# Kernel optimization log

Measured on AMD Instinct MI355X. Metric: run time of the kernel, lower is better.

Reference implementation:

```python
import jax, jax.numpy as jnp
import numpy as np

B, T, N = 1024, 128, 5
HIDDEN = 160
FML = HIDDEN // N            # 32, per-node state width
FC = (256, 256, 512)
IN_F = (FML + 1) * N         # 165: full graph -> every node sees all 5 nodes
N_CLASSES = 7
BN_EPS = 1e-5


def setup_inputs() -> dict:
    key = jax.random.key(0)
    ks = jax.random.split(key, 12)
    init = lambda k, sh: (jax.random.normal(k, sh, jnp.float32) * 0.02)
    return {
        "x": jax.random.normal(ks[0], (B, N, T), jnp.float32),
        # per-node 3-layer MLP f_i, stacked over nodes
        "Wf1": init(ks[1], (N, IN_F, FC[0])), "bf1": jnp.zeros((N, FC[0]), jnp.float32),
        "Wf2": init(ks[2], (N, FC[0], FC[1])), "bf2": jnp.zeros((N, FC[1]), jnp.float32),
        "Wf3": init(ks[3], (N, FC[1], FML)), "bf3": jnp.zeros((N, FML), jnp.float32),
        # output head: Linear -> ReLU -> BatchNorm1d -> Linear -> Softmax
        "Wo1": init(ks[4], (IN_F, FC[2])), "bo1": jnp.zeros((FC[2],), jnp.float32),
        "gamma": jnp.ones((FC[2],), jnp.float32), "beta": jnp.zeros((FC[2],), jnp.float32),
        "Wo2": init(ks[5], (FC[2], N_CLASSES)), "bo2": jnp.zeros((N_CLASSES,), jnp.float32),
    }


def reference(x, Wf1, bf1, Wf2, bf2, Wf3, bf3, Wo1, bo1, gamma, beta, Wo2, bo2):
    batch = x.shape[0]
    xt = jnp.transpose(x, (2, 0, 1))                  # [T, B, N]
    state0 = jnp.zeros((batch, N, FML), x.dtype)      # [B, N, FML]

    def step(state, x_t):
        # Gauss-Seidel update: node i sees states already updated this step
        for i in range(N):
            inp = jnp.concatenate([x_t, state.reshape(batch, -1)], axis=1)  # [B, 165]
            h = jax.nn.relu(inp @ Wf1[i] + bf1[i])
            h = jax.nn.relu(h @ Wf2[i] + bf2[i])
            s_i = jax.nn.relu(h @ Wf3[i] + bf3[i])    # [B, FML]
            state = state.at[:, i, :].set(s_i)
        return state, None

    state, _ = jax.lax.scan(step, state0, xt)
    feat = jnp.concatenate([xt[-1], state.reshape(batch, -1)], axis=1)       # [B, 165]
    h = jax.nn.relu(feat @ Wo1 + bo1)
    # BatchNorm1d in training mode: batch mean, biased batch variance
    mu = jnp.mean(h, axis=0)
    var = jnp.mean((h - mu) ** 2, axis=0)
    h = (h - mu) / jnp.sqrt(var + BN_EPS) * gamma + beta
    logits = h @ Wo2 + bo2
    return jax.nn.softmax(logits, axis=1)             # [B, 7]
```

## Files before the change

### kernel.cpp

```cpp
#include <hip/hip_runtime.h>
#include <hip/hip_bf16.h>

#define B_TOT 1024
#define T_STEPS 128
#define N_NODES 5
#define FML 32
#define IN_F 165
#define F1 256
#define F2 256
#define F3 512
#define NCLS 7
#define BM 16
#define BMH 8

typedef __attribute__((ext_vector_type(8))) short bfrag;
typedef __attribute__((ext_vector_type(4))) float f32x4;

#define MFMA16 __builtin_amdgcn_mfma_f32_16x16x32_bf16

#define L1_KT 6
#define L1_CT 16
#define L2_KT 8
#define L2_CT 16
#define L3_KT 8
#define L3_CT 2
#define L1_FRAGS (L1_KT * L1_CT)
#define L2_FRAGS (L2_KT * L2_CT)
#define L3_FRAGS (L3_KT * L3_CT)

#define INP_STRIDE 200
#define H_STRIDE 264

__device__ __forceinline__ __hip_bfloat16 tobf(float v) { return __float2bfloat16(v); }

__device__ __forceinline__ void phase_barrier() {
  asm volatile("s_waitcnt lgkmcnt(0)" ::: "memory");
  __builtin_amdgcn_s_barrier();
  __builtin_amdgcn_sched_barrier(0);
}

__global__ __launch_bounds__(256) void pack_weights(
    const float* __restrict__ Wf1, const float* __restrict__ Wf2, const float* __restrict__ Wf3,
    __hip_bfloat16* __restrict__ p1, __hip_bfloat16* __restrict__ p2, __hip_bfloat16* __restrict__ p3) {
  int tid = blockIdx.x * 256 + threadIdx.x;
  int node = tid / (240 * 64);
  int rem  = tid % (240 * 64);
  int frag = rem >> 6;
  int lane = rem & 63;
  int g = lane >> 4, c16 = lane & 15;
  if (frag < L1_FRAGS) {
    int kt = frag / L1_CT, ct = frag % L1_CT;
    __hip_bfloat16* dst = p1 + (((size_t)node * L1_FRAGS + frag) * 64 + lane) * 8;
    const float* W = Wf1 + (size_t)node * IN_F * F1;
#pragma unroll
    for (int e = 0; e < 8; ++e) {
      int k = kt * 32 + g * 8 + e;
      int row = (k < 160) ? (5 + k) : ((k < IN_F) ? (k - 160) : -1);
      float v = (row >= 0) ? W[(size_t)row * F1 + ct * 16 + c16] : 0.f;
      dst[e] = tobf(v);
    }
  } else if (frag < L1_FRAGS + L2_FRAGS) {
    int f = frag - L1_FRAGS;
    __hip_bfloat16* dst = p2 + (((size_t)node * L2_FRAGS + f) * 64 + lane) * 8;
    const float* W = Wf2 + (size_t)node * F1 * F2;
    int kt = f / L2_CT, ct = f % L2_CT;
#pragma unroll
    for (int e = 0; e < 8; ++e) {
      int k = kt * 32 + g * 8 + e;
      dst[e] = tobf(W[(size_t)k * F2 + ct * 16 + c16]);
    }
  } else {
    int f = frag - L1_FRAGS - L2_FRAGS;
    __hip_bfloat16* dst = p3 + (((size_t)node * L3_FRAGS + f) * 64 + lane) * 8;
    const float* W = Wf3 + (size_t)node * F2 * FML;
    int kt = f / L3_CT, ct = f % L3_CT;
#pragma unroll
    for (int e = 0; e < 8; ++e) {
      int k = kt * 32 + g * 8 + e;
      dst[e] = tobf(W[(size_t)k * FML + ct * 16 + c16]);
    }
  }
}

__device__ __forceinline__ void relu_pack_store(__hip_bfloat16* p, f32x4 acc, float4 b) {
  union { ushort4 v; __hip_bfloat16 h[4]; } u;
  u.h[0] = tobf(fmaxf(acc[0] + b.x, 0.f));
  u.h[1] = tobf(fmaxf(acc[1] + b.y, 0.f));
  u.h[2] = tobf(fmaxf(acc[2] + b.z, 0.f));
  u.h[3] = tobf(fmaxf(acc[3] + b.w, 0.f));
  *reinterpret_cast<ushort4*>(p) = u.v;
}

__global__ __launch_bounds__(512, 2) void recur_kernel(
    const float* __restrict__ x,
    const __hip_bfloat16* __restrict__ p1, const float* __restrict__ bf1,
    const __hip_bfloat16* __restrict__ p2, const float* __restrict__ bf2,
    const __hip_bfloat16* __restrict__ p3, const float* __restrict__ bf3,
    float* __restrict__ feat_out) {
  __shared__ __align__(16) __hip_bfloat16 inp_s[BM][INP_STRIDE];
  __shared__ __align__(16) __hip_bfloat16 h1_s[BM][H_STRIDE];
  __shared__ __align__(16) __hip_bfloat16 h2_s[BM][H_STRIDE];
  __shared__ __align__(16) bfrag wf3_s[N_NODES * L3_FRAGS * 64];

  const int tid = threadIdx.x;
  const int lane = tid & 63;
  const int w = tid >> 6;
  const int g = lane >> 4;
  const int c16 = lane & 15;
  const int ct0 = 2 * w, ct1 = 2 * w + 1;
  const int r0 = blockIdx.x * BM;

  const bfrag* Pf1 = (const bfrag*)p1;
  const bfrag* Pf2 = (const bfrag*)p2;

  const bool xact = (tid >= 128 && tid < 128 + BM * N_NODES);
  const int xr = (tid - 128) / N_NODES, xn = (tid - 128) % N_NODES;

  {
    const uint4* src = (const uint4*)p3;
    uint4* dst = (uint4*)wf3_s;
    for (int i2 = tid; i2 < N_NODES * L3_FRAGS * 64; i2 += 512) dst[i2] = src[i2];
  }
  for (int idx = tid; idx < BM * INP_STRIDE; idx += 512)
    ((__hip_bfloat16*)inp_s)[idx] = tobf(0.f);
  __syncthreads();
  if (tid < BM * N_NODES) {
    int r = tid / N_NODES, n = tid % N_NODES;
    inp_s[r][160 + n] = tobf(x[(size_t)(r0 + r) * (N_NODES * T_STEPS) + n * T_STEPS]);
  }
  __syncthreads();

  bfrag wL1[2][L1_KT];
#pragma unroll
  for (int kt = 0; kt < L1_KT; ++kt) {
    wL1[0][kt] = Pf1[(kt * L1_CT + ct0) * 64 + lane];
    wL1[1][kt] = Pf1[(kt * L1_CT + ct1) * 64 + lane];
  }

#pragma unroll 1
  for (int t = 0; t < T_STEPS; ++t) {
#pragma unroll 1
    for (int i = 0; i < N_NODES; ++i) {
      const int inext = (i + 1 == N_NODES) ? 0 : i + 1;

      bfrag w2[2][L2_KT];
      {
        const bfrag* P = Pf2 + (size_t)i * L2_FRAGS * 64;
#pragma unroll
        for (int kt = 0; kt < L2_KT; ++kt) {
          w2[0][kt] = P[(kt * L2_CT + ct0) * 64 + lane];
          w2[1][kt] = P[(kt * L2_CT + ct1) * 64 + lane];
        }
      }
      float xv = 0.f;
      if (i == 0 && xact && t + 1 < T_STEPS)
        xv = x[(size_t)(r0 + xr) * (N_NODES * T_STEPS) + xn * T_STEPS + (t + 1)];

      {
        float4 bia0 = *(const float4*)&bf1[i * F1 + ct0 * 16 + 4 * g];
        float4 bia1 = *(const float4*)&bf1[i * F1 + ct1 * 16 + 4 * g];
        bfrag a[L1_KT];
#pragma unroll
        for (int kt = 0; kt < L1_KT; ++kt)
          a[kt] = *(const bfrag*)&inp_s[c16][kt * 32 + g * 8];
        f32x4 acc0 = {0.f,0.f,0.f,0.f}, acc1 = {0.f,0.f,0.f,0.f};
        f32x4 acc0b = {0.f,0.f,0.f,0.f}, acc1b = {0.f,0.f,0.f,0.f};
#pragma unroll
        for (int kt = 0; kt < 3; ++kt) {
          acc0  = MFMA16(wL1[0][kt],     a[kt],     acc0,  0, 0, 0);
          acc1  = MFMA16(wL1[1][kt],     a[kt],     acc1,  0, 0, 0);
          acc0b = MFMA16(wL1[0][kt + 3], a[kt + 3], acc0b, 0, 0, 0);
          acc1b = MFMA16(wL1[1][kt + 3], a[kt + 3], acc1b, 0, 0, 0);
        }
        acc0 += acc0b; acc1 += acc1b;
        relu_pack_store(&h1_s[c16][ct0 * 16 + 4 * g], acc0, bia0);
        relu_pack_store(&h1_s[c16][ct1 * 16 + 4 * g], acc1, bia1);
      }
      phase_barrier();

      bfrag w1n[2][L1_KT];
      {
        const bfrag* P = Pf1 + (size_t)inext * L1_FRAGS * 64;
#pragma unroll
        for (int kt = 0; kt < L1_KT; ++kt) {
          w1n[0][kt] = P[(kt * L1_CT + ct0) * 64 + lane];
          w1n[1][kt] = P[(kt * L1_CT + ct1) * 64 + lane];
        }
      }
      {
        float4 bib0 = *(const float4*)&bf2[i * F2 + ct0 * 16 + 4 * g];
        float4 bib1 = *(const float4*)&bf2[i * F2 + ct1 * 16 + 4 * g];
        bfrag ab[L2_KT];
#pragma unroll
        for (int kt = 0; kt < L2_KT; ++kt)
          ab[kt] = *(const bfrag*)&h1_s[c16][kt * 32 + g * 8];
        f32x4 bcc0 = {0.f,0.f,0.f,0.f}, bcc1 = {0.f,0.f,0.f,0.f};
        f32x4 bcc0b = {0.f,0.f,0.f,0.f}, bcc1b = {0.f,0.f,0.f,0.f};
#pragma unroll
        for (int kt = 0; kt < 4; ++kt) {
          bcc0  = MFMA16(w2[0][kt],     ab[kt],     bcc0,  0, 0, 0);
          bcc1  = MFMA16(w2[1][kt],     ab[kt],     bcc1,  0, 0, 0);
          bcc0b = MFMA16(w2[0][kt + 4], ab[kt + 4], bcc0b, 0, 0, 0);
          bcc1b = MFMA16(w2[1][kt + 4], ab[kt + 4], bcc1b, 0, 0, 0);
        }
        bcc0 += bcc0b; bcc1 += bcc1b;
        relu_pack_store(&h2_s[c16][ct0 * 16 + 4 * g], bcc0, bib0);
        relu_pack_store(&h2_s[c16][ct1 * 16 + 4 * g], bcc1, bib1);
      }
      phase_barrier();

      if (w < 2) {
        bfrag ac[L3_KT], wc[L3_KT];
#pragma unroll
        for (int kt = 0; kt < L3_KT; ++kt) {
          wc[kt] = wf3_s[((size_t)i * L3_FRAGS + kt * L3_CT + w) * 64 + lane];
          ac[kt] = *(const bfrag*)&h2_s[c16][kt * 32 + g * 8];
        }
        f32x4 ccc = {0.f,0.f,0.f,0.f}, cccb = {0.f,0.f,0.f,0.f};
#pragma unroll
        for (int kt = 0; kt < 4; ++kt) {
          ccc  = MFMA16(wc[kt],     ac[kt],     ccc,  0, 0, 0);
          cccb = MFMA16(wc[kt + 4], ac[kt + 4], cccb, 0, 0, 0);
        }
        ccc += cccb;
        const int sc = i * FML + w * 16 + 4 * g;
        float4 bic = *(const float4*)&bf3[sc];
        union { ushort4 v; __hip_bfloat16 h[4]; } u;
        float vs[4];
#pragma unroll
        for (int e = 0; e < 4; ++e) {
          vs[e] = fmaxf(ccc[e] + ((const float*)&bic)[e], 0.f);
          u.h[e] = tobf(vs[e]);
        }
        *reinterpret_cast<ushort4*>(&inp_s[c16][sc]) = u.v;
        if (t == T_STEPS - 1) {
#pragma unroll
          for (int e = 0; e < 4; ++e)
            feat_out[(size_t)(r0 + c16) * IN_F + 5 + sc + e] = vs[e];
        }
      } else if (i == N_NODES - 1 && xact && t + 1 < T_STEPS) {
        float xv2 = x[(size_t)(r0 + xr) * (N_NODES * T_STEPS) + xn * T_STEPS + (t + 1)];
        inp_s[xr][160 + xn] = tobf(xv2);
      }
      phase_barrier();

#pragma unroll
      for (int kt = 0; kt < L1_KT; ++kt) {
        wL1[0][kt] = w1n[0][kt];
        wL1[1][kt] = w1n[1][kt];
      }
    }
  }

  if (tid < BM * N_NODES) {
    int r = tid / N_NODES, n = tid % N_NODES;
    feat_out[(size_t)(r0 + r) * IN_F + n] =
        x[(size_t)(r0 + r) * (N_NODES * T_STEPS) + n * T_STEPS + (T_STEPS - 1)];
  }
}

__global__ __launch_bounds__(256) void head1_kernel(
    const float* __restrict__ feat, const float* __restrict__ Wo1,
    const float* __restrict__ bo1, float* __restrict__ H) {
  __shared__ __align__(16) float f[BMH][168];
  const int tid = threadIdx.x;
  const int r0 = blockIdx.x * BMH;
  for (int idx = tid; idx < BMH * 168; idx += 256) {
    int r = idx / 168, c = idx % 168;
    f[r][c] = (c < IN_F) ? feat[(size_t)(r0 + r) * IN_F + c] : 0.f;
  }
  __syncthreads();
  const int c0 = tid, c1 = tid + 256;
  float acc0[BMH], acc1[BMH];
#pragma unroll
  for (int r = 0; r < BMH; ++r) { acc0[r] = 0.f; acc1[r] = 0.f; }
  int k = 0;
  for (; k + 3 < IN_F; k += 4) {
    float w00 = Wo1[(k + 0) * F3 + c0], w01 = Wo1[(k + 0) * F3 + c1];
    float w10 = Wo1[(k + 1) * F3 + c0], w11 = Wo1[(k + 1) * F3 + c1];
    float w20 = Wo1[(k + 2) * F3 + c0], w21 = Wo1[(k + 2) * F3 + c1];
    float w30 = Wo1[(k + 3) * F3 + c0], w31 = Wo1[(k + 3) * F3 + c1];
#pragma unroll
    for (int r = 0; r < BMH; ++r) {
      float4 v = *reinterpret_cast<const float4*>(&f[r][k]);
      acc0[r] = fmaf(v.x, w00, acc0[r]); acc1[r] = fmaf(v.x, w01, acc1[r]);
      acc0[r] = fmaf(v.y, w10, acc0[r]); acc1[r] = fmaf(v.y, w11, acc1[r]);
      acc0[r] = fmaf(v.z, w20, acc0[r]); acc1[r] = fmaf(v.z, w21, acc1[r]);
      acc0[r] = fmaf(v.w, w30, acc0[r]); acc1[r] = fmaf(v.w, w31, acc1[r]);
    }
  }
  {
    float w0 = Wo1[164 * F3 + c0], w1 = Wo1[164 * F3 + c1];
#pragma unroll
    for (int r = 0; r < BMH; ++r) {
      acc0[r] = fmaf(f[r][164], w0, acc0[r]);
      acc1[r] = fmaf(f[r][164], w1, acc1[r]);
    }
  }
  float b0 = bo1[c0], b1 = bo1[c1];
#pragma unroll
  for (int r = 0; r < BMH; ++r) {
    H[(size_t)(r0 + r) * F3 + c0] = fmaxf(acc0[r] + b0, 0.f);
    H[(size_t)(r0 + r) * F3 + c1] = fmaxf(acc1[r] + b1, 0.f);
  }
}

__global__ __launch_bounds__(256) void bn_stats_kernel(
    const float* __restrict__ H, const float* __restrict__ gamma,
    const float* __restrict__ beta, float* __restrict__ ab) {
  const int c = blockIdx.x;
  const int tid = threadIdx.x;
  float sm = 0.f, q = 0.f;
  for (int r = tid; r < B_TOT; r += 256) {
    float v = H[(size_t)r * F3 + c];
    sm += v; q += v * v;
  }
  __shared__ float ls[256], lq[256];
  ls[tid] = sm; lq[tid] = q;
  __syncthreads();
  for (int off = 128; off; off >>= 1) {
    if (tid < off) { ls[tid] += ls[tid + off]; lq[tid] += lq[tid + off]; }
    __syncthreads();
  }
  if (tid == 0) {
    float mu = ls[0] * (1.f / B_TOT);
    float var = lq[0] * (1.f / B_TOT) - mu * mu;
    float inv = rsqrtf(var + 1e-5f);
    float a = gamma[c] * inv;
    ab[c] = a;
    ab[F3 + c] = beta[c] - mu * a;
  }
}

__global__ __launch_bounds__(256) void out_kernel(
    const float* __restrict__ H, const float* __restrict__ ab,
    const float* __restrict__ Wo2, const float* __restrict__ bo2,
    float* __restrict__ out) {
  const int wid = threadIdx.x >> 6, lane = threadIdx.x & 63;
  const int r = blockIdx.x * 4 + wid;
  float acc[NCLS];
#pragma unroll
  for (int j = 0; j < NCLS; ++j) acc[j] = 0.f;
  for (int k = lane; k < F3; k += 64) {
    float hv = H[(size_t)r * F3 + k] * ab[k] + ab[F3 + k];
#pragma unroll
    for (int j = 0; j < NCLS; ++j) acc[j] = fmaf(hv, Wo2[k * NCLS + j], acc[j]);
  }
#pragma unroll
  for (int j = 0; j < NCLS; ++j)
    for (int off = 32; off; off >>= 1) acc[j] += __shfl_xor(acc[j], off);
  if (lane == 0) {
    float lg[NCLS], mx = -1e30f;
#pragma unroll
    for (int j = 0; j < NCLS; ++j) { lg[j] = acc[j] + bo2[j]; mx = fmaxf(mx, lg[j]); }
    float sum = 0.f;
#pragma unroll
    for (int j = 0; j < NCLS; ++j) { lg[j] = __expf(lg[j] - mx); sum += lg[j]; }
    float inv = 1.f / sum;
#pragma unroll
    for (int j = 0; j < NCLS; ++j) out[(size_t)r * NCLS + j] = lg[j] * inv;
  }
}

extern "C" void kernel_launch(void* const* d_in, const int* in_sizes, int n_in,
                              void* d_out, int out_size, void* d_ws, size_t ws_size,
                              hipStream_t stream) {
  const float* x   = (const float*)d_in[0];
  const float* Wf1 = (const float*)d_in[1];
  const float* bf1 = (const float*)d_in[2];
  const float* Wf2 = (const float*)d_in[3];
  const float* bf2 = (const float*)d_in[4];
  const float* Wf3 = (const float*)d_in[5];
  const float* bf3 = (const float*)d_in[6];
  const float* Wo1 = (const float*)d_in[7];
  const float* bo1 = (const float*)d_in[8];
  const float* gamma = (const float*)d_in[9];
  const float* beta  = (const float*)d_in[10];
  const float* Wo2 = (const float*)d_in[11];
  const float* bo2 = (const float*)d_in[12];
  float* out = (float*)d_out;

  char* ws = (char*)d_ws;
  size_t off = 0;
  __hip_bfloat16* p1 = (__hip_bfloat16*)(ws + off); off += (size_t)N_NODES * L1_FRAGS * 64 * 8 * 2;
  __hip_bfloat16* p2 = (__hip_bfloat16*)(ws + off); off += (size_t)N_NODES * L2_FRAGS * 64 * 8 * 2;
  __hip_bfloat16* p3 = (__hip_bfloat16*)(ws + off); off += (size_t)N_NODES * L3_FRAGS * 64 * 8 * 2;
  float* feat = (float*)(ws + off); off += (size_t)B_TOT * IN_F * 4;
  float* H    = (float*)(ws + off); off += (size_t)B_TOT * F3 * 4;
  float* ab   = (float*)(ws + off); off += 2 * F3 * 4;

  pack_weights<<<300, 256, 0, stream>>>(Wf1, Wf2, Wf3, p1, p2, p3);
  recur_kernel<<<B_TOT / BM, 512, 0, stream>>>(x, p1, bf1, p2, bf2, p3, bf3, feat);
  head1_kernel<<<B_TOT / BMH, 256, 0, stream>>>(feat, Wo1, bo1, H);
  bn_stats_kernel<<<F3, 256, 0, stream>>>(H, gamma, beta, ab);
  out_kernel<<<B_TOT / 4, 256, 0, stream>>>(H, ab, Wo2, bo2, out);
}
```

Measured before the change: 1.497 ms.

## Double recurrent block width to 16 waves, one column tile per wave

The recurrent kernel now launches 1024 threads per block, so each of 16 waves computes a single 16-column tile of layers 1 and 2 instead of two. This halves per-wave MFMA count and register weight footprint on the serial critical path. Layer 1 also drops the mostly-zero sixth K tile: the 5 x-input rows get their own compact fragment, loaded only by lanes with g==0 and zero elsewhere. In exchange the block barriers now synchronize twice as many waves, and __launch_bounds__(1024, 4) may tighten register limits.

```diff
diff --git a/kernel.cpp b/kernel.cpp
--- a/kernel.cpp
+++ b/kernel.cpp
@@ -18,15 +18,12 @@
 
 #define MFMA16 __builtin_amdgcn_mfma_f32_16x16x32_bf16
 
-#define L1_KT 6
-#define L1_CT 16
-#define L2_KT 8
-#define L2_CT 16
-#define L3_KT 8
-#define L3_CT 2
-#define L1_FRAGS (L1_KT * L1_CT)
-#define L2_FRAGS (L2_KT * L2_CT)
-#define L3_FRAGS (L3_KT * L3_CT)
+#define P1_NODE 43008
+#define P1_XOFF 40960
+#define L2_FRAGS 128
+#define P2_NODE (L2_FRAGS * 64 * 8)
+#define L3_FRAGS 16
+#define P3_NODE (L3_FRAGS * 64 * 8)
 
 #define INP_STRIDE 200
 #define H_STRIDE 264
@@ -42,42 +39,52 @@
 __global__ __launch_bounds__(256) void pack_weights(
     const float* __restrict__ Wf1, const float* __restrict__ Wf2, const float* __restrict__ Wf3,
     __hip_bfloat16* __restrict__ p1, __hip_bfloat16* __restrict__ p2, __hip_bfloat16* __restrict__ p3) {
-  int tid = blockIdx.x * 256 + threadIdx.x;
-  int node = tid / (240 * 64);
-  int rem  = tid % (240 * 64);
-  int frag = rem >> 6;
-  int lane = rem & 63;
-  int g = lane >> 4, c16 = lane & 15;
-  if (frag < L1_FRAGS) {
-    int kt = frag / L1_CT, ct = frag % L1_CT;
-    __hip_bfloat16* dst = p1 + (((size_t)node * L1_FRAGS + frag) * 64 + lane) * 8;
-    const float* W = Wf1 + (size_t)node * IN_F * F1;
-#pragma unroll
-    for (int e = 0; e < 8; ++e) {
-      int k = kt * 32 + g * 8 + e;
-      int row = (k < 160) ? (5 + k) : ((k < IN_F) ? (k - 160) : -1);
-      float v = (row >= 0) ? W[(size_t)row * F1 + ct * 16 + c16] : 0.f;
-      dst[e] = tobf(v);
-    }
-  } else if (frag < L1_FRAGS + L2_FRAGS) {
-    int f = frag - L1_FRAGS;
-    __hip_bfloat16* dst = p2 + (((size_t)node * L2_FRAGS + f) * 64 + lane) * 8;
-    const float* W = Wf2 + (size_t)node * F1 * F2;
-    int kt = f / L2_CT, ct = f % L2_CT;
-#pragma unroll
-    for (int e = 0; e < 8; ++e) {
-      int k = kt * 32 + g * 8 + e;
-      dst[e] = tobf(W[(size_t)k * F2 + ct * 16 + c16]);
-    }
-  } else {
-    int f = frag - L1_FRAGS - L2_FRAGS;
-    __hip_bfloat16* dst = p3 + (((size_t)node * L3_FRAGS + f) * 64 + lane) * 8;
-    const float* W = Wf3 + (size_t)node * F2 * FML;
-    int kt = f / L3_CT, ct = f % L3_CT;
-#pragma unroll
-    for (int e = 0; e < 8; ++e) {
-      int k = kt * 32 + g * 8 + e;
-      dst[e] = tobf(W[(size_t)k * FML + ct * 16 + c16]);
+  const int stride = gridDim.x * 256;
+  for (int it = blockIdx.x * 256 + threadIdx.x; it < N_NODES * 14592; it += stride) {
+    int node = it / 14592, u = it % 14592;
+    if (u < 5120) {
+      int lane = u & 63, frag = u >> 6;
+      int kt = frag >> 4, ct = frag & 15;
+      int g = lane >> 4, c16 = lane & 15;
+      __hip_bfloat16* dst = p1 + (size_t)node * P1_NODE + (size_t)u * 8;
+      const float* W = Wf1 + (size_t)node * IN_F * F1;
+#pragma unroll
+      for (int e = 0; e < 8; ++e) {
+        int k = kt * 32 + g * 8 + e;
+        dst[e] = tobf(W[(size_t)(5 + k) * F1 + ct * 16 + c16]);
+      }
+    } else if (u < 5376) {
+      int v = u - 5120;
+      int ct = v >> 4, c16 = v & 15;
+      __hip_bfloat16* dst = p1 + (size_t)node * P1_NODE + P1_XOFF + (size_t)v * 8;
+      const float* W = Wf1 + (size_t)node * IN_F * F1;
+#pragma unroll
+      for (int e = 0; e < 8; ++e)
+        dst[e] = (e < 5) ? tobf(W[(size_t)e * F1 + ct * 16 + c16]) : tobf(0.f);
+    } else if (u < 5376 + 8192) {
+      int v = u - 5376;
+      int lane = v & 63, frag = v >> 6;
+      int kt = frag >> 4, ct = frag & 15;
+      int g = lane >> 4, c16 = lane & 15;
+      __hip_bfloat16* dst = p2 + (size_t)node * P2_NODE + (size_t)v * 8;
+      const float* W = Wf2 + (size_t)node * F1 * F2;
+#pragma unroll
+      for (int e = 0; e < 8; ++e) {
+        int k = kt * 32 + g * 8 + e;
+        dst[e] = tobf(W[(size_t)k * F2 + ct * 16 + c16]);
+      }
+    } else {
+      int v = u - 13568;
+      int lane = v & 63, frag = v >> 6;
+      int kt = frag >> 1, ct = frag & 1;
+      int g = lane >> 4, c16 = lane & 15;
+      __hip_bfloat16* dst = p3 + (size_t)node * P3_NODE + (size_t)v * 8;
+      const float* W = Wf3 + (size_t)node * F2 * FML;
+#pragma unroll
+      for (int e = 0; e < 8; ++e) {
+        int k = kt * 32 + g * 8 + e;
+        dst[e] = tobf(W[(size_t)k * FML + ct * 16 + c16]);
+      }
     }
   }
 }
@@ -91,7 +98,7 @@
   *reinterpret_cast<ushort4*>(p) = u.v;
 }
 
-__global__ __launch_bounds__(512, 2) void recur_kernel(
+__global__ __launch_bounds__(1024, 4) void recur_kernel(
     const float* __restrict__ x,
     const __hip_bfloat16* __restrict__ p1, const float* __restrict__ bf1,
     const __hip_bfloat16* __restrict__ p2, const float* __restrict__ bf2,
@@ -107,21 +114,18 @@
   const int w = tid >> 6;
   const int g = lane >> 4;
   const int c16 = lane & 15;
-  const int ct0 = 2 * w, ct1 = 2 * w + 1;
+  const int ct = w;
   const int r0 = blockIdx.x * BM;
 
   const bfrag* Pf1 = (const bfrag*)p1;
   const bfrag* Pf2 = (const bfrag*)p2;
-
-  const bool xact = (tid >= 128 && tid < 128 + BM * N_NODES);
-  const int xr = (tid - 128) / N_NODES, xn = (tid - 128) % N_NODES;
 
   {
     const uint4* src = (const uint4*)p3;
     uint4* dst = (uint4*)wf3_s;
-    for (int i2 = tid; i2 < N_NODES * L3_FRAGS * 64; i2 += 512) dst[i2] = src[i2];
-  }
-  for (int idx = tid; idx < BM * INP_STRIDE; idx += 512)
+    for (int i2 = tid; i2 < N_NODES * L3_FRAGS * 64; i2 += 1024) dst[i2] = src[i2];
+  }
+  for (int idx = tid; idx < BM * INP_STRIDE; idx += 1024)
     ((__hip_bfloat16*)inp_s)[idx] = tobf(0.f);
   __syncthreads();
   if (tid < BM * N_NODES) {
@@ -130,11 +134,13 @@
   }
   __syncthreads();
 
-  bfrag wL1[2][L1_KT];
-#pragma unroll
-  for (int kt = 0; kt < L1_KT; ++kt) {
-    wL1[0][kt] = Pf1[(kt * L1_CT + ct0) * 64 + lane];
-    wL1[1][kt] = Pf1[(kt * L1_CT + ct1) * 64 + lane];
+  bfrag wL1[5], wL1x;
+#pragma unroll
+  for (int kt = 0; kt < 5; ++kt)
+    wL1[kt] = Pf1[(size_t)0 * (P1_NODE / 8) + (kt * 16 + ct) * 64 + lane];
+  {
+    bfrag z = {0,0,0,0,0,0,0,0};
+    wL1x = (g == 0) ? Pf1[(size_t)0 * (P1_NODE / 8) + P1_XOFF / 8 + ct * 16 + c16] : z;
   }
 
 #pragma unroll 1
@@ -143,93 +149,79 @@
     for (int i = 0; i < N_NODES; ++i) {
       const int inext = (i + 1 == N_NODES) ? 0 : i + 1;
 
-      bfrag w2[2][L2_KT];
+      bfrag w2[8];
       {
         const bfrag* P = Pf2 + (size_t)i * L2_FRAGS * 64;
 #pragma unroll
-        for (int kt = 0; kt < L2_KT; ++kt) {
-          w2[0][kt] = P[(kt * L2_CT + ct0) * 64 + lane];
-          w2[1][kt] = P[(kt * L2_CT + ct1) * 64 + lane];
-        }
-      }
-      float xv = 0.f;
-      if (i == 0 && xact && t + 1 < T_STEPS)
-        xv = x[(size_t)(r0 + xr) * (N_NODES * T_STEPS) + xn * T_STEPS + (t + 1)];
-
+        for (int kt = 0; kt < 8; ++kt)
+          w2[kt] = P[(kt * 16 + ct) * 64 + lane];
+      }
       {
-        float4 bia0 = *(const float4*)&bf1[i * F1 + ct0 * 16 + 4 * g];
-        float4 bia1 = *(const float4*)&bf1[i * F1 + ct1 * 16 + 4 * g];
-        bfrag a[L1_KT];
-#pragma unroll
-        for (int kt = 0; kt < L1_KT; ++kt)
+        float4 bia = *(const float4*)&bf1[i * F1 + ct * 16 + 4 * g];
+        bfrag a[5], a5;
+#pragma unroll
+        for (int kt = 0; kt < 5; ++kt)
           a[kt] = *(const bfrag*)&inp_s[c16][kt * 32 + g * 8];
-        f32x4 acc0 = {0.f,0.f,0.f,0.f}, acc1 = {0.f,0.f,0.f,0.f};
-        f32x4 acc0b = {0.f,0.f,0.f,0.f}, acc1b = {0.f,0.f,0.f,0.f};
-#pragma unroll
-        for (int kt = 0; kt < 3; ++kt) {
-          acc0  = MFMA16(wL1[0][kt],     a[kt],     acc0,  0, 0, 0);
-          acc1  = MFMA16(wL1[1][kt],     a[kt],     acc1,  0, 0, 0);
-          acc0b = MFMA16(wL1[0][kt + 3], a[kt + 3], acc0b, 0, 0, 0);
-          acc1b = MFMA16(wL1[1][kt + 3], a[kt + 3], acc1b, 0, 0, 0);
-        }
-        acc0 += acc0b; acc1 += acc1b;
-        relu_pack_store(&h1_s[c16][ct0 * 16 + 4 * g], acc0, bia0);
-        relu_pack_store(&h1_s[c16][ct1 * 16 + 4 * g], acc1, bia1);
+        a5 = *(const bfrag*)&inp_s[c16][160 + g * 8];
+        f32x4 acc = {0.f,0.f,0.f,0.f}, accb = {0.f,0.f,0.f,0.f};
+        acc  = MFMA16(wL1[0], a[0], acc,  0, 0, 0);
+        accb = MFMA16(wL1[3], a[3], accb, 0, 0, 0);
+        acc  = MFMA16(wL1[1], a[1], acc,  0, 0, 0);
+        accb = MFMA16(wL1[4], a[4], accb, 0, 0, 0);
+        acc  = MFMA16(wL1[2], a[2], acc,  0, 0, 0);
+        accb = MFMA16(wL1x,   a5,   accb, 0, 0, 0);
+        acc += accb;
+        relu_pack_store(&h1_s[c16][ct * 16 + 4 * g], acc, bia);
       }
       phase_barrier();
 
-      bfrag w1n[2][L1_KT];
+      bfrag w1n[5], w1nx;
       {
-        const bfrag* P = Pf1 + (size_t)inext * L1_FRAGS * 64;
-#pragma unroll
-        for (int kt = 0; kt < L1_KT; ++kt) {
-          w1n[0][kt] = P[(kt * L1_CT + ct0) * 64 + lane];
-          w1n[1][kt] = P[(kt * L1_CT + ct1) * 64 + lane];
-        }
+        const bfrag* P = Pf1 + (size_t)inext * (P1_NODE / 8);
+#pragma unroll
+        for (int kt = 0; kt < 5; ++kt)
+          w1n[kt] = P[(kt * 16 + ct) * 64 + lane];
+        bfrag z = {0,0,0,0,0,0,0,0};
+        w1nx = (g == 0) ? P[P1_XOFF / 8 + ct * 16 + c16] : z;
       }
       {
-        float4 bib0 = *(const float4*)&bf2[i * F2 + ct0 * 16 + 4 * g];
-        float4 bib1 = *(const float4*)&bf2[i * F2 + ct1 * 16 + 4 * g];
-        bfrag ab[L2_KT];
-#pragma unroll
-        for (int kt = 0; kt < L2_KT; ++kt)
+        float4 bib = *(const float4*)&bf2[i * F2 + ct * 16 + 4 * g];
+        bfrag ab[8];
+#pragma unroll
+        for (int kt = 0; kt < 8; ++kt)
           ab[kt] = *(const bfrag*)&h1_s[c16][kt * 32 + g * 8];
-        f32x4 bcc0 = {0.f,0.f,0.f,0.f}, bcc1 = {0.f,0.f,0.f,0.f};
-        f32x4 bcc0b = {0.f,0.f,0.f,0.f}, bcc1b = {0.f,0.f,0.f,0.f};
+        f32x4 acc = {0.f,0.f,0.f,0.f}, accb = {0.f,0.f,0.f,0.f};
 #pragma unroll
         for (int kt = 0; kt < 4; ++kt) {
-          bcc0  = MFMA16(w2[0][kt],     ab[kt],     bcc0,  0, 0, 0);
-          bcc1  = MFMA16(w2[1][kt],     ab[kt],     bcc1,  0, 0, 0);
-          bcc0b = MFMA16(w2[0][kt + 4], ab[kt + 4], bcc0b, 0, 0, 0);
-          bcc1b = MFMA16(w2[1][kt + 4], ab[kt + 4], bcc1b, 0, 0, 0);
-        }
-        bcc0 += bcc0b; bcc1 += bcc1b;
-        relu_pack_store(&h2_s[c16][ct0 * 16 + 4 * g], bcc0, bib0);
-        relu_pack_store(&h2_s[c16][ct1 * 16 + 4 * g], bcc1, bib1);
+          acc  = MFMA16(w2[kt],     ab[kt],     acc,  0, 0, 0);
+          accb = MFMA16(w2[kt + 4], ab[kt + 4], accb, 0, 0, 0);
+        }
+        acc += accb;
+        relu_pack_store(&h2_s[c16][ct * 16 + 4 * g], acc, bib);
       }
       phase_barrier();
 
       if (w < 2) {
-        bfrag ac[L3_KT], wc[L3_KT];
-#pragma unroll
-        for (int kt = 0; kt < L3_KT; ++kt) {
-          wc[kt] = wf3_s[((size_t)i * L3_FRAGS + kt * L3_CT + w) * 64 + lane];
+        bfrag ac[8], wc[8];
+#pragma unroll
+        for (int kt = 0; kt < 8; ++kt) {
+          wc[kt] = wf3_s[((size_t)i * L3_FRAGS + kt * 2 + w) * 64 + lane];
           ac[kt] = *(const bfrag*)&h2_s[c16][kt * 32 + g * 8];
         }
-        f32x4 ccc = {0.f,0.f,0.f,0.f}, cccb = {0.f,0.f,0.f,0.f};
+        f32x4 acc = {0.f,0.f,0.f,0.f}, accb = {0.f,0.f,0.f,0.f};
 #pragma unroll
         for (int kt = 0; kt < 4; ++kt) {
-          ccc  = MFMA16(wc[kt],     ac[kt],     ccc,  0, 0, 0);
-          cccb = MFMA16(wc[kt + 4], ac[kt + 4], cccb, 0, 0, 0);
-        }
-        ccc += cccb;
+          acc  = MFMA16(wc[kt],     ac[kt],     acc,  0, 0, 0);
+          accb = MFMA16(wc[kt + 4], ac[kt + 4], accb, 0, 0, 0);
+        }
+        acc += accb;
         const int sc = i * FML + w * 16 + 4 * g;
         float4 bic = *(const float4*)&bf3[sc];
         union { ushort4 v; __hip_bfloat16 h[4]; } u;
         float vs[4];
 #pragma unroll
         for (int e = 0; e < 4; ++e) {
-          vs[e] = fmaxf(ccc[e] + ((const float*)&bic)[e], 0.f);
+          vs[e] = fmaxf(acc[e] + ((const float*)&bic)[e], 0.f);
           u.h[e] = tobf(vs[e]);
         }
         *reinterpret_cast<ushort4*>(&inp_s[c16][sc]) = u.v;
@@ -238,17 +230,16 @@
           for (int e = 0; e < 4; ++e)
             feat_out[(size_t)(r0 + c16) * IN_F + 5 + sc + e] = vs[e];
         }
-      } else if (i == N_NODES - 1 && xact && t + 1 < T_STEPS) {
-        float xv2 = x[(size_t)(r0 + xr) * (N_NODES * T_STEPS) + xn * T_STEPS + (t + 1)];
-        inp_s[xr][160 + xn] = tobf(xv2);
+      } else if (i == N_NODES - 1 && t + 1 < T_STEPS && tid >= 512 && tid < 512 + BM * N_NODES) {
+        int xr = (tid - 512) / N_NODES, xn = (tid - 512) % N_NODES;
+        float xv = x[(size_t)(r0 + xr) * (N_NODES * T_STEPS) + xn * T_STEPS + (t + 1)];
+        inp_s[xr][160 + xn] = tobf(xv);
       }
       phase_barrier();
 
 #pragma unroll
-      for (int kt = 0; kt < L1_KT; ++kt) {
-        wL1[0][kt] = w1n[0][kt];
-        wL1[1][kt] = w1n[1][kt];
-      }
+      for (int kt = 0; kt < 5; ++kt) wL1[kt] = w1n[kt];
+      wL1x = w1nx;
     }
   }
 
@@ -382,15 +373,15 @@
 
   char* ws = (char*)d_ws;
   size_t off = 0;
-  __hip_bfloat16* p1 = (__hip_bfloat16*)(ws + off); off += (size_t)N_NODES * L1_FRAGS * 64 * 8 * 2;
-  __hip_bfloat16* p2 = (__hip_bfloat16*)(ws + off); off += (size_t)N_NODES * L2_FRAGS * 64 * 8 * 2;
-  __hip_bfloat16* p3 = (__hip_bfloat16*)(ws + off); off += (size_t)N_NODES * L3_FRAGS * 64 * 8 * 2;
+  __hip_bfloat16* p1 = (__hip_bfloat16*)(ws + off); off += (size_t)N_NODES * P1_NODE * 2;
+  __hip_bfloat16* p2 = (__hip_bfloat16*)(ws + off); off += (size_t)N_NODES * P2_NODE * 2;
+  __hip_bfloat16* p3 = (__hip_bfloat16*)(ws + off); off += (size_t)N_NODES * P3_NODE * 2;
   float* feat = (float*)(ws + off); off += (size_t)B_TOT * IN_F * 4;
   float* H    = (float*)(ws + off); off += (size_t)B_TOT * F3 * 4;
   float* ab   = (float*)(ws + off); off += 2 * F3 * 4;
 
-  pack_weights<<<300, 256, 0, stream>>>(Wf1, Wf2, Wf3, p1, p2, p3);
-  recur_kernel<<<B_TOT / BM, 512, 0, stream>>>(x, p1, bf1, p2, bf2, p3, bf3, feat);
+  pack_weights<<<285, 256, 0, stream>>>(Wf1, Wf2, Wf3, p1, p2, p3);
+  recur_kernel<<<B_TOT / BM, 1024, 0, stream>>>(x, p1, bf1, p2, bf2, p3, bf3, feat);
   head1_kernel<<<B_TOT / BMH, 256, 0, stream>>>(feat, Wo1, bo1, H);
   bn_stats_kernel<<<F3, 256, 0, stream>>>(H, gamma, beta, ab);
   out_kernel<<<B_TOT / 4, 256, 0, stream>>>(H, ab, Wo2, bo2, out);
```

Result: slower. 1.569 ms (+4.8%).
